# Kernel optimization log

Hardware: AMD Instinct MI355X
Metric: run time of the kernel (lower is better)

The kernel has to match this reference:

```python
import jax, jax.numpy as jnp
import numpy as np

EPS = 1e-5

def _layernorm(h, g, b):
    mu = jnp.mean(h, axis=-1, keepdims=True)
    var = jnp.mean(jnp.square(h - mu), axis=-1, keepdims=True)
    return (h - mu) * jax.lax.rsqrt(var + EPS) * g + b

def setup_inputs() -> dict:
    key = jax.random.key(0)
    ks = jax.random.split(key, 16)
    N, E, H = 100000, 500000, 128
    x = jax.random.normal(ks[0], (N, H), dtype=jnp.float32)
    edge_index = jax.random.randint(ks[1], (2, E), 0, N, dtype=jnp.int64)
    edge = jax.random.normal(ks[2], (E, H), dtype=jnp.float32)
    def lin(k, fan_in, fan_out):
        bound = 1.0 / np.sqrt(fan_in)
        k1, k2 = jax.random.split(k)
        W = jax.random.uniform(k1, (fan_in, fan_out), jnp.float32, -bound, bound)
        b = jax.random.uniform(k2, (fan_out,), jnp.float32, -bound, bound)
        return W, b
    W0, b0 = lin(ks[3], 3 * H, H)
    W1, b1 = lin(ks[4], H, H)
    W2, b2 = lin(ks[5], H, H)
    W3, b3 = lin(ks[6], H, 1)
    g0 = jnp.ones((H,), jnp.float32); be0 = jnp.zeros((H,), jnp.float32)
    g1 = jnp.ones((H,), jnp.float32); be1 = jnp.zeros((H,), jnp.float32)
    g2 = jnp.ones((H,), jnp.float32); be2 = jnp.zeros((H,), jnp.float32)
    return dict(x=x, edge_index=edge_index, edge=edge,
                W0=W0, b0=b0, g0=g0, be0=be0,
                W1=W1, b1=b1, g1=g1, be1=be1,
                W2=W2, b2=b2, g2=g2, be2=be2,
                W3=W3, b3=b3)

def reference(x, edge_index, edge, W0, b0, g0, be0, W1, b1, g1, be1, W2, b2, g2, be2, W3, b3):
    src, dst = edge_index[0], edge_index[1]
    # gather + concat: [E, 3*H]
    h = jnp.concatenate([x[src], x[dst], edge], axis=-1)
    h = jax.nn.relu(_layernorm(h @ W0 + b0, g0, be0))
    h = jax.nn.relu(_layernorm(h @ W1 + b1, g1, be1))
    h = jax.nn.relu(_layernorm(h @ W2 + b2, g2, be2))
    out = h @ W3 + b3  # [E, 1]
    return jnp.squeeze(out, axis=-1)
```

## Files before the change

kernel.cpp:

```cpp
#include <hip/hip_runtime.h>

typedef _Float16 f16;
typedef _Float16 f16x8 __attribute__((ext_vector_type(8)));
typedef _Float16 f16x4 __attribute__((ext_vector_type(4)));
typedef float    f32x4 __attribute__((ext_vector_type(4)));

static constexpr int H  = 128;
static constexpr int MT = 128;
static constexpr int PC = 40;

__device__ __forceinline__ void wg_barrier() {
    asm volatile("s_waitcnt lgkmcnt(0)" ::: "memory");
    __builtin_amdgcn_s_barrier();
    asm volatile("" ::: "memory");
}

__global__ __launch_bounds__(256, 3)
void edge_mlp_fused(const float* __restrict__ x,
                    const int* __restrict__ eidx,
                    const float* __restrict__ edge,
                    const float* __restrict__ W0, const float* __restrict__ b0,
                    const float* __restrict__ g0, const float* __restrict__ be0,
                    const float* __restrict__ W1, const float* __restrict__ b1,
                    const float* __restrict__ g1, const float* __restrict__ be1,
                    const float* __restrict__ W2, const float* __restrict__ b2,
                    const float* __restrict__ g2, const float* __restrict__ be2,
                    const float* __restrict__ W3, const float* __restrict__ b3,
                    float* __restrict__ out, int E)
{
    __shared__ __align__(16) f16 achunk[MT * PC];
    __shared__ __align__(16) f16 wchunk[H * PC];
    __shared__ __align__(16) f16 act[MT * H];

    const int tid  = threadIdx.x;
    const int lane = tid & 63;
    const int wid  = tid >> 6;
    const int c    = lane & 15;
    const int g    = lane >> 4;
    const int wrow = wid * 32;
    const long long e0 = (long long)blockIdx.x * MT;

    const int srow = tid >> 1;
    const int hf   = tid & 1;
    long long er = e0 + srow; if (er >= E) er = (long long)E - 1;
    const float* psrc = x    + (size_t)eidx[er]     * H + hf * 16;
    const float* pdst = x    + (size_t)eidx[E + er] * H + hf * 16;
    const float* pedg = edge + (size_t)er           * H + hf * 16;

    f32x4 acc[8][2];
    #pragma unroll
    for (int t = 0; t < 8; ++t) {
        acc[t][0] = f32x4{0.f, 0.f, 0.f, 0.f};
        acc[t][1] = f32x4{0.f, 0.f, 0.f, 0.f};
    }

    float4 apf0, apf1, apf2, apf3;
    float  wpf[16];

    auto issueA = [&](int kc) {
        const float* b = (kc < 4) ? psrc : (kc < 8) ? pdst : pedg;
        const float4* p = (const float4*)(b + (kc & 3) * 32);
        apf0 = p[0]; apf1 = p[1]; apf2 = p[2]; apf3 = p[3];
    };
    auto writeA = [&]() {
        f16x8 lo, hi;
        lo[0] = (f16)apf0.x; lo[1] = (f16)apf0.y; lo[2] = (f16)apf0.z; lo[3] = (f16)apf0.w;
        lo[4] = (f16)apf1.x; lo[5] = (f16)apf1.y; lo[6] = (f16)apf1.z; lo[7] = (f16)apf1.w;
        hi[0] = (f16)apf2.x; hi[1] = (f16)apf2.y; hi[2] = (f16)apf2.z; hi[3] = (f16)apf2.w;
        hi[4] = (f16)apf3.x; hi[5] = (f16)apf3.y; hi[6] = (f16)apf3.z; hi[7] = (f16)apf3.w;
        *(f16x8*)&achunk[srow * PC + hf * 16]     = lo;
        *(f16x8*)&achunk[srow * PC + hf * 16 + 8] = hi;
    };
    auto issueW = [&](const float* __restrict__ W, int k0) {
        #pragma unroll
        for (int i = 0; i < 4; ++i) {
            int f  = i * 256 + tid;
            int n  = f & 127;
            int kq = f >> 7;
            const float* p = W + (size_t)(k0 + kq * 4) * H + n;
            wpf[i * 4 + 0] = p[0];
            wpf[i * 4 + 1] = p[H];
            wpf[i * 4 + 2] = p[2 * H];
            wpf[i * 4 + 3] = p[3 * H];
        }
    };
    auto writeW = [&]() {
        #pragma unroll
        for (int i = 0; i < 4; ++i) {
            int f  = i * 256 + tid;
            int n  = f & 127;
            int kq = f >> 7;
            f16x4 v;
            v[0] = (f16)wpf[i * 4 + 0];
            v[1] = (f16)wpf[i * 4 + 1];
            v[2] = (f16)wpf[i * 4 + 2];
            v[3] = (f16)wpf[i * 4 + 3];
            *(f16x4*)&wchunk[n * PC + kq * 4] = v;
        }
    };

    auto mfma_ach = [&]() {
        f16x8 a0 = *(const f16x8*)&achunk[(wrow + c)      * PC + g * 8];
        f16x8 a1 = *(const f16x8*)&achunk[(wrow + 16 + c) * PC + g * 8];
        #pragma unroll
        for (int t = 0; t < 8; ++t) {
            f16x8 bf = *(const f16x8*)&wchunk[(t * 16 + c) * PC + g * 8];
            acc[t][0] = __builtin_amdgcn_mfma_f32_16x16x32_f16(a0, bf, acc[t][0], 0, 0, 0);
            acc[t][1] = __builtin_amdgcn_mfma_f32_16x16x32_f16(a1, bf, acc[t][1], 0, 0, 0);
        }
    };
    auto mfma_act = [&](int koff) {
        int col = (koff + g * 8) ^ ((c & 7) << 3);
        f16x8 a0 = *(const f16x8*)&act[(wrow + c)      * H + col];
        f16x8 a1 = *(const f16x8*)&act[(wrow + 16 + c) * H + col];
        #pragma unroll
        for (int t = 0; t < 8; ++t) {
            f16x8 bf = *(const f16x8*)&wchunk[(t * 16 + c) * PC + g * 8];
            acc[t][0] = __builtin_amdgcn_mfma_f32_16x16x32_f16(a0, bf, acc[t][0], 0, 0, 0);
            acc[t][1] = __builtin_amdgcn_mfma_f32_16x16x32_f16(a1, bf, acc[t][1], 0, 0, 0);
        }
    };

    auto ln_relu_store = [&](const float* __restrict__ bias,
                             const float* __restrict__ gamma,
                             const float* __restrict__ beta) {
        float mu[2][4], rs[2][4];
        #pragma unroll
        for (int t = 0; t < 8; ++t) {
            float bt = bias[t * 16 + c];
            #pragma unroll
            for (int s = 0; s < 2; ++s)
                #pragma unroll
                for (int r = 0; r < 4; ++r) acc[t][s][r] += bt;
        }
        #pragma unroll
        for (int s = 0; s < 2; ++s)
            #pragma unroll
            for (int r = 0; r < 4; ++r) {
                float v = 0.f, q = 0.f;
                #pragma unroll
                for (int t = 0; t < 8; ++t) { float a = acc[t][s][r]; v += a; q += a * a; }
                #pragma unroll
                for (int m = 1; m < 16; m <<= 1) {
                    v += __shfl_xor(v, m, 64);
                    q += __shfl_xor(q, m, 64);
                }
                float mean = v * (1.0f / H);
                float var  = q * (1.0f / H) - mean * mean;
                mu[s][r] = mean;
                rs[s][r] = rsqrtf(var + 1e-5f);
            }
        #pragma unroll
        for (int t = 0; t < 8; ++t) {
            float gm = gamma[t * 16 + c];
            float bb = beta[t * 16 + c];
            #pragma unroll
            for (int s = 0; s < 2; ++s)
                #pragma unroll
                for (int r = 0; r < 4; ++r) {
                    float v = (acc[t][s][r] - mu[s][r]) * rs[s][r] * gm + bb;
                    v = fmaxf(v, 0.f);
                    int row = wrow + s * 16 + g * 4 + r;
                    act[row * H + ((t * 16 + c) ^ ((row & 7) << 3))] = (f16)v;
                }
        }
        #pragma unroll
        for (int t = 0; t < 8; ++t) {
            acc[t][0] = f32x4{0.f, 0.f, 0.f, 0.f};
            acc[t][1] = f32x4{0.f, 0.f, 0.f, 0.f};
        }
    };

    issueA(0);
    issueW(W0, 0);
    #pragma unroll 1
    for (int kc = 0; kc < 12; ++kc) {
        wg_barrier();
        writeA();
        writeW();
        if (kc < 11) { issueA(kc + 1); issueW(W0, (kc + 1) * 32); }
        else         { issueW(W1, 0); }
        wg_barrier();
        mfma_ach();
    }
    ln_relu_store(b0, g0, be0);

    #pragma unroll 1
    for (int kc = 0; kc < 4; ++kc) {
        wg_barrier();
        writeW();
        if (kc < 3) issueW(W1, (kc + 1) * 32);
        else        issueW(W2, 0);
        wg_barrier();
        mfma_act(kc * 32);
    }
    ln_relu_store(b1, g1, be1);

    #pragma unroll 1
    for (int kc = 0; kc < 4; ++kc) {
        wg_barrier();
        writeW();
        if (kc < 3) issueW(W2, (kc + 1) * 32);
        wg_barrier();
        mfma_act(kc * 32);
    }

    {
        float mu[2][4], rs[2][4];
        #pragma unroll
        for (int t = 0; t < 8; ++t) {
            float bt = b2[t * 16 + c];
            #pragma unroll
            for (int s = 0; s < 2; ++s)
                #pragma unroll
                for (int r = 0; r < 4; ++r) acc[t][s][r] += bt;
        }
        #pragma unroll
        for (int s = 0; s < 2; ++s)
            #pragma unroll
            for (int r = 0; r < 4; ++r) {
                float v = 0.f, q = 0.f;
                #pragma unroll
                for (int t = 0; t < 8; ++t) { float a = acc[t][s][r]; v += a; q += a * a; }
                #pragma unroll
                for (int m = 1; m < 16; m <<= 1) {
                    v += __shfl_xor(v, m, 64);
                    q += __shfl_xor(q, m, 64);
                }
                float mean = v * (1.0f / H);
                float var  = q * (1.0f / H) - mean * mean;
                mu[s][r] = mean;
                rs[s][r] = rsqrtf(var + 1e-5f);
            }
        float po[2][4] = {{0.f,0.f,0.f,0.f},{0.f,0.f,0.f,0.f}};
        #pragma unroll
        for (int t = 0; t < 8; ++t) {
            float gm  = g2[t * 16 + c];
            float bb  = be2[t * 16 + c];
            float w3v = W3[t * 16 + c];
            #pragma unroll
            for (int s = 0; s < 2; ++s)
                #pragma unroll
                for (int r = 0; r < 4; ++r) {
                    float v = (acc[t][s][r] - mu[s][r]) * rs[s][r] * gm + bb;
                    v = fmaxf(v, 0.f);
                    po[s][r] += v * w3v;
                }
        }
        #pragma unroll
        for (int s = 0; s < 2; ++s)
            #pragma unroll
            for (int r = 0; r < 4; ++r) {
                #pragma unroll
                for (int m = 1; m < 16; m <<= 1) po[s][r] += __shfl_xor(po[s][r], m, 64);
            }
        if (c == 0) {
            float bb3 = b3[0];
            #pragma unroll
            for (int s = 0; s < 2; ++s) {
                long long eb = e0 + wrow + s * 16 + g * 4;
                if (eb + 3 < E) {
                    float4 o;
                    o.x = po[s][0] + bb3; o.y = po[s][1] + bb3;
                    o.z = po[s][2] + bb3; o.w = po[s][3] + bb3;
                    *(float4*)(out + eb) = o;
                } else {
                    #pragma unroll
                    for (int r = 0; r < 4; ++r)
                        if (eb + r < E) out[eb + r] = po[s][r] + bb3;
                }
            }
        }
    }
}

extern "C" void kernel_launch(void* const* d_in, const int* in_sizes, int n_in,
                              void* d_out, int out_size, void* d_ws, size_t ws_size,
                              hipStream_t stream)
{
    const float* x    = (const float*)d_in[0];
    const int*   eidx = (const int*)d_in[1];
    const float* edge = (const float*)d_in[2];
    const float* W0   = (const float*)d_in[3];
    const float* b0   = (const float*)d_in[4];
    const float* g0   = (const float*)d_in[5];
    const float* be0  = (const float*)d_in[6];
    const float* W1   = (const float*)d_in[7];
    const float* b1   = (const float*)d_in[8];
    const float* g1   = (const float*)d_in[9];
    const float* be1  = (const float*)d_in[10];
    const float* W2   = (const float*)d_in[11];
    const float* b2   = (const float*)d_in[12];
    const float* g2   = (const float*)d_in[13];
    const float* be2  = (const float*)d_in[14];
    const float* W3   = (const float*)d_in[15];
    const float* b3   = (const float*)d_in[16];
    float*       out  = (float*)d_out;

    const int E = in_sizes[1] / 2;
    const int grid = (E + MT - 1) / MT;

    hipLaunchKernelGGL(edge_mlp_fused, dim3(grid), dim3(256), 0, stream,
                       x, eidx, edge,
                       W0, b0, g0, be0,
                       W1, b1, g1, be1,
                       W2, b2, g2, be2,
                       W3, b3, out, E);
}
```

Baseline: 681.9 us.

## Pre-convert weights to fp16 workspace and double-buffer via direct global-to-LDS loads

Adds a prep kernel that converts W0/W1/W2 to fp16 in a swizzled chunk layout in the workspace. The main kernel then streams each weight chunk straight into a double-buffered LDS slot with global_load_lds, so the two barriers per k-step become one. Each wave now gathers only its own 32 edge rows into a private LDS slice, and the activation buffer shares that storage. The aim is to remove per-block fp32 weight loads and conversions and to overlap weight staging with MFMA work, at the cost of an extra small launch and more LDS for the double buffer.

```diff
diff --git a/kernel.cpp b/kernel.cpp
--- a/kernel.cpp
+++ b/kernel.cpp
@@ -5,20 +5,42 @@
 typedef _Float16 f16x4 __attribute__((ext_vector_type(4)));
 typedef float    f32x4 __attribute__((ext_vector_type(4)));
 
-static constexpr int H  = 128;
-static constexpr int MT = 128;
-static constexpr int PC = 40;
-
-__device__ __forceinline__ void wg_barrier() {
-    asm volatile("s_waitcnt lgkmcnt(0)" ::: "memory");
-    __builtin_amdgcn_s_barrier();
-    asm volatile("" ::: "memory");
+static constexpr int H   = 128;
+static constexpr int MT  = 128;
+static constexpr int WCH = 4096;
+static constexpr int NCH = 20;
+static constexpr size_t WS_NEED = (size_t)NCH * WCH * sizeof(f16);
+
+__global__ __launch_bounds__(256)
+void wprep(const float* __restrict__ W0, const float* __restrict__ W1,
+           const float* __restrict__ W2, f16* __restrict__ ws)
+{
+    int e = blockIdx.x * 256 + threadIdx.x;
+    if (e >= NCH * WCH) return;
+    int cid = e >> 12;
+    int rem = e & 4095;
+    int k   = rem >> 7;
+    int n   = rem & 127;
+    const float* W; int k0;
+    if (cid < 12)      { W = W0; k0 = cid * 32; }
+    else if (cid < 16) { W = W1; k0 = (cid - 12) * 32; }
+    else               { W = W2; k0 = (cid - 16) * 32; }
+    f16 v = (f16)W[(size_t)(k0 + k) * H + n];
+    int su = (k >> 3) ^ ((n >> 2) & 3);
+    ws[cid * WCH + n * 32 + su * 8 + (k & 7)] = v;
 }
 
+__device__ __forceinline__ void glds16(const f16* g, f16* l) {
+    __builtin_amdgcn_global_load_lds((const __attribute__((address_space(1))) void*)g,
+                                     (__attribute__((address_space(3))) void*)l, 16, 0, 0);
+}
+
+template <int WPRE>
 __global__ __launch_bounds__(256, 3)
 void edge_mlp_fused(const float* __restrict__ x,
                     const int* __restrict__ eidx,
                     const float* __restrict__ edge,
+                    const f16* __restrict__ wpre,
                     const float* __restrict__ W0, const float* __restrict__ b0,
                     const float* __restrict__ g0, const float* __restrict__ be0,
                     const float* __restrict__ W1, const float* __restrict__ b1,
@@ -28,9 +50,8 @@
                     const float* __restrict__ W3, const float* __restrict__ b3,
                     float* __restrict__ out, int E)
 {
-    __shared__ __align__(16) f16 achunk[MT * PC];
-    __shared__ __align__(16) f16 wchunk[H * PC];
-    __shared__ __align__(16) f16 act[MT * H];
+    __shared__ __align__(16) f16 wch[2 * WCH];
+    __shared__ __align__(16) f16 uni[MT * H];
 
     const int tid  = threadIdx.x;
     const int lane = tid & 63;
@@ -40,12 +61,18 @@
     const int wrow = wid * 32;
     const long long e0 = (long long)blockIdx.x * MT;
 
-    const int srow = tid >> 1;
-    const int hf   = tid & 1;
-    long long er = e0 + srow; if (er >= E) er = (long long)E - 1;
-    const float* psrc = x    + (size_t)eidx[er]     * H + hf * 16;
-    const float* pdst = x    + (size_t)eidx[E + er] * H + hf * 16;
-    const float* pedg = edge + (size_t)er           * H + hf * 16;
+    const int r_ = lane >> 1;
+    const int hf = lane & 1;
+    long long er = e0 + wrow + r_; if (er >= E) er = (long long)E - 1;
+    const float* psrc = x    + (size_t)eidx[er]     * H;
+    const float* pdst = x    + (size_t)eidx[E + er] * H;
+    const float* pedg = edge + (size_t)er           * H;
+
+    f16* aslice = &uni[wid * 1024];
+    const int s_    = (r_ >> 2) & 3;
+    const int aoff0 = r_ * 32 + ((2 * hf)     ^ s_) * 8;
+    const int aoff1 = r_ * 32 + ((2 * hf + 1) ^ s_) * 8;
+    const int sw    = (g ^ ((c >> 2) & 3)) * 8;
 
     f32x4 acc[8][2];
     #pragma unroll
@@ -55,11 +82,9 @@
     }
 
     float4 apf0, apf1, apf2, apf3;
-    float  wpf[16];
-
     auto issueA = [&](int kc) {
-        const float* b = (kc < 4) ? psrc : (kc < 8) ? pdst : pedg;
-        const float4* p = (const float4*)(b + (kc & 3) * 32);
+        const float* bptr = (kc < 4) ? psrc : (kc < 8) ? pdst : pedg;
+        const float4* p = (const float4*)(bptr + (kc & 3) * 32 + hf * 16);
         apf0 = p[0]; apf1 = p[1]; apf2 = p[2]; apf3 = p[3];
     };
     auto writeA = [&]() {
@@ -68,54 +93,53 @@
         lo[4] = (f16)apf1.x; lo[5] = (f16)apf1.y; lo[6] = (f16)apf1.z; lo[7] = (f16)apf1.w;
         hi[0] = (f16)apf2.x; hi[1] = (f16)apf2.y; hi[2] = (f16)apf2.z; hi[3] = (f16)apf2.w;
         hi[4] = (f16)apf3.x; hi[5] = (f16)apf3.y; hi[6] = (f16)apf3.z; hi[7] = (f16)apf3.w;
-        *(f16x8*)&achunk[srow * PC + hf * 16]     = lo;
-        *(f16x8*)&achunk[srow * PC + hf * 16 + 8] = hi;
-    };
-    auto issueW = [&](const float* __restrict__ W, int k0) {
-        #pragma unroll
-        for (int i = 0; i < 4; ++i) {
-            int f  = i * 256 + tid;
-            int n  = f & 127;
-            int kq = f >> 7;
-            const float* p = W + (size_t)(k0 + kq * 4) * H + n;
-            wpf[i * 4 + 0] = p[0];
-            wpf[i * 4 + 1] = p[H];
-            wpf[i * 4 + 2] = p[2 * H];
-            wpf[i * 4 + 3] = p[3 * H];
-        }
-    };
-    auto writeW = [&]() {
-        #pragma unroll
-        for (int i = 0; i < 4; ++i) {
-            int f  = i * 256 + tid;
-            int n  = f & 127;
-            int kq = f >> 7;
-            f16x4 v;
-            v[0] = (f16)wpf[i * 4 + 0];
-            v[1] = (f16)wpf[i * 4 + 1];
-            v[2] = (f16)wpf[i * 4 + 2];
-            v[3] = (f16)wpf[i * 4 + 3];
-            *(f16x4*)&wchunk[n * PC + kq * 4] = v;
-        }
-    };
-
-    auto mfma_ach = [&]() {
-        f16x8 a0 = *(const f16x8*)&achunk[(wrow + c)      * PC + g * 8];
-        f16x8 a1 = *(const f16x8*)&achunk[(wrow + 16 + c) * PC + g * 8];
-        #pragma unroll
-        for (int t = 0; t < 8; ++t) {
-            f16x8 bf = *(const f16x8*)&wchunk[(t * 16 + c) * PC + g * 8];
+        *(f16x8*)&aslice[aoff0] = lo;
+        *(f16x8*)&aslice[aoff1] = hi;
+    };
+
+    auto stageW = [&](int cid, int pbuf) {
+        f16* dst = &wch[pbuf * WCH];
+        if (WPRE) {
+            const f16* src = wpre + (size_t)cid * WCH + wid * 1024;
+            f16* d = dst + wid * 1024;
+            glds16(src + (lane << 3), d);
+            glds16(src + 512 + (lane << 3), d + 512);
+        } else {
+            const float* W = (cid < 12) ? W0 : (cid < 16) ? W1 : W2;
+            int k0 = ((cid < 12) ? cid : (cid < 16) ? (cid - 12) : (cid - 16)) * 32;
+            #pragma unroll
+            for (int i = 0; i < 4; ++i) {
+                int f  = i * 256 + tid;
+                int n  = f & 127;
+                int kq = f >> 7;
+                const float* pw = W + (size_t)(k0 + kq * 4) * H + n;
+                f16x4 v;
+                v[0] = (f16)pw[0]; v[1] = (f16)pw[H]; v[2] = (f16)pw[2 * H]; v[3] = (f16)pw[3 * H];
+                int su = (kq >> 1) ^ ((n >> 2) & 3);
+                *(f16x4*)&dst[n * 32 + su * 8 + (kq & 1) * 4] = v;
+            }
+        }
+    };
+
+    auto mfma_ach = [&](int pbuf) {
+        const f16* wb = &wch[pbuf * WCH];
+        f16x8 a0 = *(const f16x8*)&aslice[c * 32 + sw];
+        f16x8 a1 = *(const f16x8*)&aslice[(16 + c) * 32 + sw];
+        #pragma unroll
+        for (int t = 0; t < 8; ++t) {
+            f16x8 bf = *(const f16x8*)&wb[(t * 16 + c) * 32 + sw];
             acc[t][0] = __builtin_amdgcn_mfma_f32_16x16x32_f16(a0, bf, acc[t][0], 0, 0, 0);
             acc[t][1] = __builtin_amdgcn_mfma_f32_16x16x32_f16(a1, bf, acc[t][1], 0, 0, 0);
         }
     };
-    auto mfma_act = [&](int koff) {
+    auto mfma_act = [&](int koff, int pbuf) {
+        const f16* wb = &wch[pbuf * WCH];
         int col = (koff + g * 8) ^ ((c & 7) << 3);
-        f16x8 a0 = *(const f16x8*)&act[(wrow + c)      * H + col];
-        f16x8 a1 = *(const f16x8*)&act[(wrow + 16 + c) * H + col];
-        #pragma unroll
-        for (int t = 0; t < 8; ++t) {
-            f16x8 bf = *(const f16x8*)&wchunk[(t * 16 + c) * PC + g * 8];
+        f16x8 a0 = *(const f16x8*)&uni[(wrow + c) * H + col];
+        f16x8 a1 = *(const f16x8*)&uni[(wrow + 16 + c) * H + col];
+        #pragma unroll
+        for (int t = 0; t < 8; ++t) {
+            f16x8 bf = *(const f16x8*)&wb[(t * 16 + c) * 32 + sw];
             acc[t][0] = __builtin_amdgcn_mfma_f32_16x16x32_f16(a0, bf, acc[t][0], 0, 0, 0);
             acc[t][1] = __builtin_amdgcn_mfma_f32_16x16x32_f16(a1, bf, acc[t][1], 0, 0, 0);
         }
@@ -161,7 +185,7 @@
                     float v = (acc[t][s][r] - mu[s][r]) * rs[s][r] * gm + bb;
                     v = fmaxf(v, 0.f);
                     int row = wrow + s * 16 + g * 4 + r;
-                    act[row * H + ((t * 16 + c) ^ ((row & 7) << 3))] = (f16)v;
+                    uni[row * H + ((t * 16 + c) ^ ((row & 7) << 3))] = (f16)v;
                 }
         }
         #pragma unroll
@@ -171,38 +195,33 @@
         }
     };
 
+    stageW(0, 0);
     issueA(0);
-    issueW(W0, 0);
-    #pragma unroll 1
+    __syncthreads();
+
+    #pragma unroll 2
     for (int kc = 0; kc < 12; ++kc) {
-        wg_barrier();
+        stageW(kc + 1, (kc + 1) & 1);
         writeA();
-        writeW();
-        if (kc < 11) { issueA(kc + 1); issueW(W0, (kc + 1) * 32); }
-        else         { issueW(W1, 0); }
-        wg_barrier();
-        mfma_ach();
+        if (kc < 11) issueA(kc + 1);
+        mfma_ach(kc & 1);
+        __syncthreads();
     }
     ln_relu_store(b0, g0, be0);
 
-    #pragma unroll 1
+    #pragma unroll 2
     for (int kc = 0; kc < 4; ++kc) {
-        wg_barrier();
-        writeW();
-        if (kc < 3) issueW(W1, (kc + 1) * 32);
-        else        issueW(W2, 0);
-        wg_barrier();
-        mfma_act(kc * 32);
+        stageW(13 + kc, (kc + 1) & 1);
+        mfma_act(kc * 32, kc & 1);
+        __syncthreads();
     }
     ln_relu_store(b1, g1, be1);
 
-    #pragma unroll 1
+    #pragma unroll 2
     for (int kc = 0; kc < 4; ++kc) {
-        wg_barrier();
-        writeW();
-        if (kc < 3) issueW(W2, (kc + 1) * 32);
-        wg_barrier();
-        mfma_act(kc * 32);
+        if (kc < 3) stageW(17 + kc, (kc + 1) & 1);
+        mfma_act(kc * 32, kc & 1);
+        if (kc < 3) __syncthreads();
     }
 
     {
@@ -300,10 +319,18 @@
     const int E = in_sizes[1] / 2;
     const int grid = (E + MT - 1) / MT;
 
-    hipLaunchKernelGGL(edge_mlp_fused, dim3(grid), dim3(256), 0, stream,
-                       x, eidx, edge,
-                       W0, b0, g0, be0,
-                       W1, b1, g1, be1,
-                       W2, b2, g2, be2,
-                       W3, b3, out, E);
+    if (d_ws && ws_size >= WS_NEED) {
+        f16* wsp = (f16*)d_ws;
+        hipLaunchKernelGGL(wprep, dim3((NCH * WCH + 255) / 256), dim3(256), 0, stream,
+                           W0, W1, W2, wsp);
+        hipLaunchKernelGGL((edge_mlp_fused<1>), dim3(grid), dim3(256), 0, stream,
+                           x, eidx, edge, (const f16*)wsp,
+                           W0, b0, g0, be0, W1, b1, g1, be1, W2, b2, g2, be2,
+                           W3, b3, out, E);
+    } else {
+        hipLaunchKernelGGL((edge_mlp_fused<0>), dim3(grid), dim3(256), 0, stream,
+                           x, eidx, edge, (const f16*)nullptr,
+                           W0, b0, g0, be0, W1, b1, g1, be1, W2, b2, g2, be2,
+                           W3, b3, out, E);
+    }
 }
```

Result: faster. 603.7 us (-11.5%).
